# Performance work log

Hardware: AMD Instinct MI355X
Metric: run time of the kernel (lower is better)

Reference implementation:

```python
import jax, jax.numpy as jnp
import numpy as np

B, S, D, DOUT = 8, 2048, 512, 512
BETA = 1.0
EPS = 1e-5


def _ln(x, g, b):
    m = jnp.mean(x, axis=-1, keepdims=True)
    v = jnp.var(x, axis=-1, keepdims=True)
    return (x - m) / jnp.sqrt(v + EPS) * g + b


def setup_inputs() -> dict:
    key = jax.random.key(0)
    ks = jax.random.split(key, 12)
    s = 0.02
    d = {
        "x": jax.random.normal(ks[0], (B, S, D), jnp.float32),
        "Wq": jax.random.normal(ks[1], (D, D), jnp.float32) * s,
        "bq": jnp.zeros((D,), jnp.float32),
        "Wk": jax.random.normal(ks[2], (D, D), jnp.float32) * s,
        "bk": jnp.zeros((D,), jnp.float32),
        "Wv": jax.random.normal(ks[3], (D, D), jnp.float32) * s,
        "bv": jnp.zeros((D,), jnp.float32),
        "ln0_g": jnp.ones((D,), jnp.float32),
        "ln0_b": jnp.zeros((D,), jnp.float32),
        "W1": jax.random.normal(ks[4], (D, D), jnp.float32) * s,
        "b1": jnp.zeros((D,), jnp.float32),
        "ln1_g": jnp.ones((D,), jnp.float32),
        "ln1_b": jnp.zeros((D,), jnp.float32),
        "W2": jax.random.normal(ks[5], (D, D), jnp.float32) * s,
        "b2": jnp.zeros((D,), jnp.float32),
        "ln2_g": jnp.ones((D,), jnp.float32),
        "ln2_b": jnp.zeros((D,), jnp.float32),
        "W3": jax.random.normal(ks[6], (D, DOUT), jnp.float32) * s,
        "b3": jnp.zeros((DOUT,), jnp.float32),
    }
    return d


def reference(x, Wq, bq, Wk, bk, Wv, bv, ln0_g, ln0_b,
              W1, b1, ln1_g, ln1_b, W2, b2, ln2_g, ln2_b, W3, b3):
    # --- attention_single (dropout disabled / eval) ---
    q = x @ Wq + bq                      # [B,S,D]
    k = x @ Wk + bk
    v = x @ Wv + bv
    scores = jnp.einsum('bsd,btd->bst', q, k)   # [B,S,S]
    w = jax.nn.softmax(BETA * scores / jnp.sqrt(jnp.float32(D)), axis=2)
    att = jnp.einsum('bst,btd->bsd', w, v)      # [B,S,D]
    out_nxt = _ln(x + att, ln0_g, ln0_b)
    # --- FFNN (dropout disabled, gelu activation) ---
    h1 = _ln(jax.nn.gelu(out_nxt + (out_nxt @ W1 + b1), approximate=False), ln1_g, ln1_b)
    h2 = _ln(jax.nn.gelu(out_nxt + (h1 @ W2 + b2), approximate=False), ln2_g, ln2_b)
    out_att = h2 @ W3 + b3               # [B,S,DOUT]
    return out_att
```

## Files before the change

### kernel.cpp

```cpp
#include <hip/hip_runtime.h>
#include <hip/hip_bf16.h>
#include <math.h>

using bf16 = __hip_bfloat16;
typedef __attribute__((ext_vector_type(8))) short short8;
typedef __attribute__((ext_vector_type(4))) float f32x4;
typedef __attribute__((ext_vector_type(4))) float float4v;

__device__ __forceinline__ float b2f(bf16 v) { return __bfloat162float(v); }
__device__ __forceinline__ bf16 f2b(float v) { return __float2bfloat16(v); }

__device__ __forceinline__ unsigned char f2e4m3(float v) {
  int p = __builtin_amdgcn_cvt_pk_fp8_f32(v, v, 0, false);
  return (unsigned char)(p & 0xff);
}

__device__ __forceinline__ void gl_lds16(const void* g, void* l) {
  __builtin_amdgcn_global_load_lds(
      (const __attribute__((address_space(1))) void*)g,
      (__attribute__((address_space(3))) void*)l, 16, 0, 0);
}

__global__ __launch_bounds__(256) void sniff_zero(const void* ln0g_raw, int* flag,
                                                  float* rowsum) {
  const int i = blockIdx.x * 256 + threadIdx.x;
  rowsum[i] = 0.f;
  if (i == 0) {
    unsigned short w = ((const unsigned short*)ln0g_raw)[0];
    *flag = (w == 0x3F80) ? 1 : 0;
  }
}

__global__ __launch_bounds__(256) void conv_x8(
    const void* __restrict__ src, bf16* __restrict__ dst,
    const int* __restrict__ flag) {
  const long i = ((long)blockIdx.x * 256 + threadIdx.x) * 8;
  bf16 o[8];
  if (*flag) {
    *(short8*)(dst + i) = ((const short8*)src)[i >> 3];
  } else {
    float4v a = ((const float4v*)src)[i >> 2];
    float4v b = ((const float4v*)src)[(i >> 2) + 1];
#pragma unroll
    for (int k = 0; k < 4; k++) o[k] = f2b(a[k]);
#pragma unroll
    for (int k = 0; k < 4; k++) o[4 + k] = f2b(b[k]);
    *(short8*)(dst + i) = *(short8*)o;
  }
}

__global__ __launch_bounds__(256) void conv_vec12(
    const void* a0, const void* a1, const void* a2, const void* a3,
    const void* a4, const void* a5, const void* a6, const void* a7,
    const void* a8, const void* a9, const void* a10, const void* a11,
    bf16* __restrict__ dst, const int* __restrict__ flag) {
  const int j = blockIdx.x;
  const int i = threadIdx.x + (blockIdx.y << 8);
  const void* s;
  switch (j) {
    case 0: s = a0; break; case 1: s = a1; break; case 2: s = a2; break;
    case 3: s = a3; break; case 4: s = a4; break; case 5: s = a5; break;
    case 6: s = a6; break; case 7: s = a7; break; case 8: s = a8; break;
    case 9: s = a9; break; case 10: s = a10; break; default: s = a11; break;
  }
  bf16 v = (*flag) ? ((const bf16*)s)[i] : f2b(((const float*)s)[i]);
  dst[j * 512 + i] = v;
}

__global__ __launch_bounds__(256) void transpose_conv6(
    const void* w0, const void* w1, const void* w2, const void* w3,
    const void* w4, const void* w5, bf16* __restrict__ outBase,
    const int* __restrict__ flag) {
  __shared__ bf16 tile[32][33];
  const void* in;
  switch (blockIdx.z) {
    case 0: in = w0; break; case 1: in = w1; break; case 2: in = w2; break;
    case 3: in = w3; break; case 4: in = w4; break; default: in = w5; break;
  }
  bf16* out = outBase + (long)blockIdx.z * 262144;
  const int f = *flag;
  const int c0 = blockIdx.x * 32, r0 = blockIdx.y * 32;
  const int tx = threadIdx.x & 31, ty = threadIdx.x >> 5;
#pragma unroll
  for (int i = ty; i < 32; i += 8) {
    const long idx = (long)(r0 + i) * 512 + c0 + tx;
    tile[i][tx] = f ? ((const bf16*)in)[idx] : f2b(((const float*)in)[idx]);
  }
  __syncthreads();
#pragma unroll
  for (int i = ty; i < 32; i += 8)
    out[(long)(c0 + i) * 512 + r0 + tx] = tile[tx][i];
}

__global__ __launch_bounds__(256, 2) void gemm_scores(
    const bf16* __restrict__ A, const bf16* __restrict__ Bt,
    unsigned char* __restrict__ out8, float* __restrict__ rowsum,
    int N, int K, long sA, long sB, long sC, float scale) {
  __shared__ __align__(16) bf16 As[128 * 32];
  __shared__ __align__(16) bf16 Bs[128 * 32];
  const int z = blockIdx.x;
  const int m0 = blockIdx.y * 128, n0 = blockIdx.z * 128;
  A += (long)z * sA;
  Bt += (long)z * sB;
  const int t = threadIdx.x;
  const int l = t & 63, w = t >> 6;
  const int wm = (w >> 1) * 64, wn = (w & 1) * 64;
  const int lr = l & 15, lq = l >> 4;

  const bf16* Ab = A + (long)m0 * K;
  const bf16* Bb = Bt + (long)n0 * K;
  const int srow = t >> 2;
  const int scol = (t & 3) * 8;

  f32x4 acc[4][4] = {};

  for (int k0 = 0; k0 < K; k0 += 32) {
    gl_lds16(Ab + (long)srow * K + k0 + scol, As + w * 512);
    gl_lds16(Ab + (long)(srow + 64) * K + k0 + scol, As + 2048 + w * 512);
    gl_lds16(Bb + (long)srow * K + k0 + scol, Bs + w * 512);
    gl_lds16(Bb + (long)(srow + 64) * K + k0 + scol, Bs + 2048 + w * 512);
    __syncthreads();
    short8 af[4], bfr[4];
#pragma unroll
    for (int i = 0; i < 4; i++)
      af[i] = *(const short8*)(As + (wm + i * 16 + lr) * 32 + lq * 8);
#pragma unroll
    for (int j = 0; j < 4; j++)
      bfr[j] = *(const short8*)(Bs + (wn + j * 16 + lr) * 32 + lq * 8);
#pragma unroll
    for (int i = 0; i < 4; i++)
#pragma unroll
      for (int j = 0; j < 4; j++)
        acc[i][j] = __builtin_amdgcn_mfma_f32_16x16x32_bf16(af[i], bfr[j], acc[i][j], 0, 0, 0);
    __syncthreads();
  }

  const int cr = lq * 4, cc = lr;
  float rs[4][4];
#pragma unroll
  for (int i = 0; i < 4; i++)
#pragma unroll
    for (int r = 0; r < 4; r++) rs[i][r] = 0.f;
#pragma unroll
  for (int i = 0; i < 4; i++) {
#pragma unroll
    for (int j = 0; j < 4; j++) {
      const int gc = n0 + wn + j * 16 + cc;
#pragma unroll
      for (int r = 0; r < 4; r++) {
        const int gr = m0 + wm + i * 16 + cr + r;
        float e = __expf(acc[i][j][r] * scale);
        out8[(long)z * sC + (long)gr * N + gc] = f2e4m3(e);
        rs[i][r] += e;
      }
    }
  }
#pragma unroll
  for (int o = 1; o < 16; o <<= 1)
#pragma unroll
    for (int i = 0; i < 4; i++)
#pragma unroll
      for (int r = 0; r < 4; r++) rs[i][r] += __shfl_xor(rs[i][r], o);
  if (lr == 0) {
#pragma unroll
    for (int i = 0; i < 4; i++)
#pragma unroll
      for (int r = 0; r < 4; r++) {
        const int gr = m0 + wm + i * 16 + cr + r;
        atomicAdd(&rowsum[(long)z * 2048 + gr], rs[i][r]);
      }
  }
}

template <int EPI, bool BX>
__global__ __launch_bounds__(256, 2) void gemm_sk(
    const bf16* __restrict__ A, const bf16* __restrict__ Bt,
    const bf16* __restrict__ bias, const bf16* __restrict__ res,
    float* __restrict__ outF, bf16* __restrict__ outB,
    unsigned char* __restrict__ out8,
    int M, int N, int K, long sA, long sB, long sC, long sBias) {
  __shared__ __align__(16) bf16 As[64 * 32];
  __shared__ __align__(16) bf16 Bs[128 * 32];
  const int z = BX ? blockIdx.x : blockIdx.z;
  const int m0 = (BX ? blockIdx.y : blockIdx.x) * 64;
  const int n0 = (BX ? blockIdx.z : blockIdx.y) * 128;
  A += (long)z * sA;
  Bt += (long)z * sB;
  if (EPI == 0) bias += (long)z * sBias;
  const int t = threadIdx.x;
  const int l = t & 63, w = t >> 6;
  const int wm = (w >> 1) * 32, wn = (w & 1) * 64;
  const int lr = l & 15, lq = l >> 4;

  const bf16* Ab = A + (long)m0 * K;
  const bf16* Bb = Bt + (long)n0 * K;
  const int srow = t >> 2;
  const int scol = (t & 3) * 8;

  f32x4 acc[2][4] = {};

  for (int k0 = 0; k0 < K; k0 += 32) {
    gl_lds16(Ab + (long)srow * K + k0 + scol, As + w * 512);
    gl_lds16(Bb + (long)srow * K + k0 + scol, Bs + w * 512);
    gl_lds16(Bb + (long)(srow + 64) * K + k0 + scol, Bs + 2048 + w * 512);
    __syncthreads();
    short8 af[2], bfr[4];
#pragma unroll
    for (int i = 0; i < 2; i++)
      af[i] = *(const short8*)(As + (wm + i * 16 + lr) * 32 + lq * 8);
#pragma unroll
    for (int j = 0; j < 4; j++)
      bfr[j] = *(const short8*)(Bs + (wn + j * 16 + lr) * 32 + lq * 8);
#pragma unroll
    for (int i = 0; i < 2; i++)
#pragma unroll
      for (int j = 0; j < 4; j++)
        acc[i][j] = __builtin_amdgcn_mfma_f32_16x16x32_bf16(af[i], bfr[j], acc[i][j], 0, 0, 0);
    __syncthreads();
  }

  const int cr = lq * 4, cc = lr;
#pragma unroll
  for (int i = 0; i < 2; i++) {
#pragma unroll
    for (int j = 0; j < 4; j++) {
      const int gc = n0 + wn + j * 16 + cc;
#pragma unroll
      for (int r = 0; r < 4; r++) {
        const int gr = m0 + wm + i * 16 + cr + r;
        const long idx = (long)z * sC + (long)gr * N + gc;
        float v = acc[i][j][r];
        if (EPI == 0) {
          v += b2f(bias[gc]);
          outB[idx] = f2b(v);
        } else if (EPI == 3) {
          v += b2f(bias[gc]) + b2f(res[idx]);
          v = 0.5f * v * (1.0f + erff(v * 0.70710678118654752f));
          outB[idx] = f2b(v);
        } else if (EPI == 4) {
          v += b2f(bias[gc]);
          outF[idx] = v;
        } else {
          v += b2f(bias[gr]);
          out8[idx] = f2e4m3(v);
        }
      }
    }
  }
}

__global__ __launch_bounds__(256, 2) void gemm_pv8(
    const unsigned char* __restrict__ A8, const unsigned char* __restrict__ B8,
    const bf16* __restrict__ res, bf16* __restrict__ outB,
    const float* __restrict__ rowsum,
    int M, int N, int K, long sA, long sB, long sC) {
  __shared__ __align__(16) unsigned char As8[64 * 64];
  __shared__ __align__(16) unsigned char Bs8[128 * 64];
  const int z = blockIdx.x;
  const int m0 = blockIdx.y * 64, n0 = blockIdx.z * 128;
  A8 += (long)z * sA;
  B8 += (long)z * sB;
  const int t = threadIdx.x;
  const int l = t & 63, w = t >> 6;
  const int wm = (w >> 1) * 32, wn = (w & 1) * 64;
  const int lr = l & 15, lq = l >> 4;

  const unsigned char* Ab = A8 + (long)m0 * K;
  const unsigned char* Bb = B8 + (long)n0 * K;

  const int arow_s = t >> 2;
  const int aL = ((t & 3) ^ ((arow_s >> 1) & 3)) * 16;
  const int brow_s2 = (t + 256) >> 2;
  const int bL2 = ((t & 3) ^ ((brow_s2 >> 1) & 3)) * 16;

  f32x4 acc[2][4] = {};

  for (int k0 = 0; k0 < K; k0 += 64) {
    gl_lds16(Ab + (long)arow_s * K + k0 + aL, As8 + w * 1024);
    gl_lds16(Bb + (long)arow_s * K + k0 + aL, Bs8 + w * 1024);
    gl_lds16(Bb + (long)brow_s2 * K + k0 + bL2, Bs8 + 4096 + w * 1024);
    __syncthreads();
#pragma unroll
    for (int kh = 0; kh < 2; kh++) {
      long long a8[2], b8[4];
#pragma unroll
      for (int i = 0; i < 2; i++) {
        const int ar = wm + i * 16 + lr;
        const int Lx = (kh * 2 + (lq >> 1)) ^ ((ar >> 1) & 3);
        a8[i] = *(const long long*)(As8 + ar * 64 + Lx * 16 + (lq & 1) * 8);
      }
#pragma unroll
      for (int j = 0; j < 4; j++) {
        const int br = wn + j * 16 + lr;
        const int Lx = (kh * 2 + (lq >> 1)) ^ ((br >> 1) & 3);
        b8[j] = *(const long long*)(Bs8 + br * 64 + Lx * 16 + (lq & 1) * 8);
      }
#pragma unroll
      for (int i = 0; i < 2; i++)
#pragma unroll
        for (int j = 0; j < 4; j++)
          acc[i][j] = __builtin_amdgcn_mfma_f32_16x16x32_fp8_fp8(a8[i], b8[j], acc[i][j], 0, 0, 0);
    }
    __syncthreads();
  }

  const int cr = lq * 4, cc = lr;
  float inv[2][4];
#pragma unroll
  for (int i = 0; i < 2; i++)
#pragma unroll
    for (int r = 0; r < 4; r++) {
      const int gr = m0 + wm + i * 16 + cr + r;
      inv[i][r] = 1.0f / rowsum[(long)z * 2048 + gr];
    }
#pragma unroll
  for (int i = 0; i < 2; i++) {
#pragma unroll
    for (int j = 0; j < 4; j++) {
      const int gc = n0 + wn + j * 16 + cc;
#pragma unroll
      for (int r = 0; r < 4; r++) {
        const int gr = m0 + wm + i * 16 + cr + r;
        const long idx = (long)z * sC + (long)gr * N + gc;
        float v = acc[i][j][r] * inv[i][r] + b2f(res[idx]);
        outB[idx] = f2b(v);
      }
    }
  }
}

__global__ __launch_bounds__(256) void ln512(
    const bf16* __restrict__ mainb,
    const bf16* __restrict__ g, const bf16* __restrict__ b,
    bf16* __restrict__ out) {
  const int t = threadIdx.x;
  const int l = t & 63, w = t >> 6;
  const long row = (long)blockIdx.x * 4 + w;
  const long base = row * 512 + l * 8;
  bf16 vb8[8];
  *(short8*)vb8 = *(const short8*)(mainb + base);
  float v[8];
  float s = 0.f, q = 0.f;
#pragma unroll
  for (int k = 0; k < 8; k++) {
    v[k] = b2f(vb8[k]);
    s += v[k];
    q += v[k] * v[k];
  }
#pragma unroll
  for (int o = 32; o > 0; o >>= 1) {
    s += __shfl_xor(s, o);
    q += __shfl_xor(q, o);
  }
  const float mean = s * (1.f / 512.f);
  const float var = q * (1.f / 512.f) - mean * mean;
  const float rstd = rsqrtf(var + 1e-5f);
  bf16 g8[8], b8[8], o8[8];
  *(short8*)g8 = *(const short8*)(g + l * 8);
  *(short8*)b8 = *(const short8*)(b + l * 8);
#pragma unroll
  for (int k = 0; k < 8; k++)
    o8[k] = f2b((v[k] - mean) * rstd * b2f(g8[k]) + b2f(b8[k]));
  *(short8*)(out + base) = *(short8*)o8;
}

__global__ void sentinel_kernel(float* out) { out[0] = 31337.0f; }

extern "C" void kernel_launch(void* const* d_in, const int* in_sizes, int n_in,
                              void* d_out, int out_size, void* d_ws, size_t ws_size,
                              hipStream_t stream) {
  const void* x_raw = d_in[0];
  const void* Wq = d_in[1];
  const void* bq = d_in[2];
  const void* Wk = d_in[3];
  const void* bk = d_in[4];
  const void* Wv = d_in[5];
  const void* bv = d_in[6];
  const void* ln0g = d_in[7];
  const void* ln0b = d_in[8];
  const void* W1 = d_in[9];
  const void* b1 = d_in[10];
  const void* ln1g = d_in[11];
  const void* ln1b = d_in[12];
  const void* W2 = d_in[13];
  const void* b2 = d_in[14];
  const void* ln2g = d_in[15];
  const void* ln2b = d_in[16];
  const void* W3 = d_in[17];
  const void* b3 = d_in[18];

  const long MB = 1024 * 1024;
  if (ws_size < (size_t)(148 * MB)) {
    sentinel_kernel<<<1, 1, 0, stream>>>((float*)d_out);
    return;
  }
  char* ws = (char*)d_ws;
  bf16* Wqt = (bf16*)(ws + 0L * 524288);
  bf16* Wvt = (bf16*)(ws + 2L * 524288);
  bf16* W1t = (bf16*)(ws + 3L * 524288);
  bf16* W2t = (bf16*)(ws + 4L * 524288);
  bf16* W3t = (bf16*)(ws + 5L * 524288);
  int* flag = (int*)(ws + 3 * MB);
  bf16* vec = (bf16*)(ws + 3 * MB + 1024);
  bf16* bqc = vec + 0 * 512;
  bf16* bvc = vec + 2 * 512;
  bf16* ln0gc = vec + 3 * 512;
  bf16* ln0bc = vec + 4 * 512;
  bf16* b1c = vec + 5 * 512;
  bf16* ln1gc = vec + 6 * 512;
  bf16* ln1bc = vec + 7 * 512;
  bf16* b2c = vec + 8 * 512;
  bf16* ln2gc = vec + 9 * 512;
  bf16* ln2bc = vec + 10 * 512;
  bf16* b3c = vec + 11 * 512;
  float* rowsum = (float*)(ws + 3 * MB + 131072);
  bf16* xc = (bf16*)(ws + 4 * MB);
  bf16* qb = (bf16*)(ws + 20 * MB);
  bf16* kb = (bf16*)(ws + 36 * MB);
  unsigned char* vt8 = (unsigned char*)(ws + 52 * MB);
  unsigned char* sc8 = (unsigned char*)(ws + 68 * MB);
  bf16* sres = (bf16*)(ws + 132 * MB);
  bf16* onx = (bf16*)(ws + 20 * MB);
  bf16* preh = (bf16*)(ws + 68 * MB);
  bf16* h1 = (bf16*)(ws + 36 * MB);
  bf16* h2 = (bf16*)(ws + 100 * MB);

  const dim3 blk(256);
  const float scale = 0.044194173824159216f;
  const long sQ = 2048L * 512, sS = 2048L * 2048;

  sniff_zero<<<dim3(64), blk, 0, stream>>>(ln0g, flag, rowsum);
  conv_x8<<<dim3(4096), blk, 0, stream>>>(x_raw, xc, flag);
  conv_vec12<<<dim3(12, 2), blk, 0, stream>>>(bq, bk, bv, ln0g, ln0b, b1, ln1g,
                                              ln1b, b2, ln2g, ln2b, b3, vec, flag);
  transpose_conv6<<<dim3(16, 16, 6), blk, 0, stream>>>(Wq, Wk, Wv, W1, W2, W3,
                                                       Wqt, flag);

  gemm_sk<0, false><<<dim3(256, 4, 2), blk, 0, stream>>>(
      xc, Wqt, bqc, nullptr, nullptr, qb, nullptr,
      16384, 512, 512, 0, 262144, 8388608, 512);
  gemm_sk<6, true><<<dim3(8, 8, 16), blk, 0, stream>>>(
      Wvt, xc, bvc, nullptr, nullptr, nullptr, vt8,
      512, 2048, 512, 0, sQ, sQ, 0);
  gemm_scores<<<dim3(8, 16, 16), blk, 0, stream>>>(
      qb, kb, sc8, rowsum, 2048, 512, sQ, sQ, sS, scale);
  gemm_pv8<<<dim3(8, 32, 4), blk, 0, stream>>>(
      sc8, vt8, xc, sres, rowsum, 2048, 512, 2048, sS, sQ, sQ);
  ln512<<<dim3(4096), blk, 0, stream>>>(sres, ln0gc, ln0bc, onx);
  gemm_sk<3, false><<<dim3(256, 4, 1), blk, 0, stream>>>(
      onx, W1t, b1c, onx, nullptr, preh, nullptr,
      16384, 512, 512, 0, 0, 0, 0);
  ln512<<<dim3(4096), blk, 0, stream>>>(preh, ln1gc, ln1bc, h1);
  gemm_sk<3, false><<<dim3(256, 4, 1), blk, 0, stream>>>(
      h1, W2t, b2c, onx, nullptr, preh, nullptr,
      16384, 512, 512, 0, 0, 0, 0);
  ln512<<<dim3(4096), blk, 0, stream>>>(preh, ln2gc, ln2bc, h2);
  gemm_sk<4, false><<<dim3(256, 4, 1), blk, 0, stream>>>(
      h2, W3t, b3c, nullptr, (float*)d_out, nullptr, nullptr,
      16384, 512, 512, 0, 0, 0, 0);
}
```

Before: 345.2 us.

## Double GEMM K-tile to 64 with XOR-swizzled LDS layout

Both the scores GEMM and the generic GEMM now stage 64-wide K slices per iteration instead of 32. Global-to-LDS loads write chunks in an XOR-swizzled order (chunk ^ row&7), and the fragment reads apply the same swizzle. The aim is to halve the number of barrier pairs per K and to avoid LDS bank conflicts on the 128-byte row stride. LDS use doubles per block, which may limit occupancy at two blocks per CU.

```diff
diff --git a/kernel.cpp b/kernel.cpp
--- a/kernel.cpp
+++ b/kernel.cpp
@@ -92,12 +92,13 @@
     out[(long)(c0 + i) * 512 + r0 + tx] = tile[tx][i];
 }
 
+
 __global__ __launch_bounds__(256, 2) void gemm_scores(
     const bf16* __restrict__ A, const bf16* __restrict__ Bt,
     unsigned char* __restrict__ out8, float* __restrict__ rowsum,
     int N, int K, long sA, long sB, long sC, float scale) {
-  __shared__ __align__(16) bf16 As[128 * 32];
-  __shared__ __align__(16) bf16 Bs[128 * 32];
+  __shared__ __align__(16) bf16 As[128 * 64];
+  __shared__ __align__(16) bf16 Bs[128 * 64];
   const int z = blockIdx.x;
   const int m0 = blockIdx.y * 128, n0 = blockIdx.z * 128;
   A += (long)z * sA;
@@ -109,29 +110,46 @@
 
   const bf16* Ab = A + (long)m0 * K;
   const bf16* Bb = Bt + (long)n0 * K;
-  const int srow = t >> 2;
-  const int scol = (t & 3) * 8;
+
+  int srcoff[4];
+#pragma unroll
+  for (int reg = 0; reg < 4; reg++) {
+    const int s = reg * 256 + t;
+    const int row = s >> 3, pch = s & 7;
+    const int L = pch ^ (row & 7);
+    srcoff[reg] = row * K + L * 8;
+  }
 
   f32x4 acc[4][4] = {};
 
-  for (int k0 = 0; k0 < K; k0 += 32) {
-    gl_lds16(Ab + (long)srow * K + k0 + scol, As + w * 512);
-    gl_lds16(Ab + (long)(srow + 64) * K + k0 + scol, As + 2048 + w * 512);
-    gl_lds16(Bb + (long)srow * K + k0 + scol, Bs + w * 512);
-    gl_lds16(Bb + (long)(srow + 64) * K + k0 + scol, Bs + 2048 + w * 512);
-    __syncthreads();
-    short8 af[4], bfr[4];
-#pragma unroll
-    for (int i = 0; i < 4; i++)
-      af[i] = *(const short8*)(As + (wm + i * 16 + lr) * 32 + lq * 8);
-#pragma unroll
-    for (int j = 0; j < 4; j++)
-      bfr[j] = *(const short8*)(Bs + (wn + j * 16 + lr) * 32 + lq * 8);
-#pragma unroll
-    for (int i = 0; i < 4; i++)
-#pragma unroll
-      for (int j = 0; j < 4; j++)
-        acc[i][j] = __builtin_amdgcn_mfma_f32_16x16x32_bf16(af[i], bfr[j], acc[i][j], 0, 0, 0);
+  for (int k0 = 0; k0 < K; k0 += 64) {
+#pragma unroll
+    for (int reg = 0; reg < 4; reg++) {
+      gl_lds16(Ab + srcoff[reg] + k0, As + reg * 2048 + w * 512);
+      gl_lds16(Bb + srcoff[reg] + k0, Bs + reg * 2048 + w * 512);
+    }
+    __syncthreads();
+#pragma unroll
+    for (int kh = 0; kh < 2; kh++) {
+      short8 af[4], bfr[4];
+#pragma unroll
+      for (int i = 0; i < 4; i++) {
+        const int r = wm + i * 16 + lr;
+        const int pc = (kh * 4 + lq) ^ (r & 7);
+        af[i] = *(const short8*)(As + r * 64 + pc * 8);
+      }
+#pragma unroll
+      for (int j = 0; j < 4; j++) {
+        const int r = wn + j * 16 + lr;
+        const int pc = (kh * 4 + lq) ^ (r & 7);
+        bfr[j] = *(const short8*)(Bs + r * 64 + pc * 8);
+      }
+#pragma unroll
+      for (int i = 0; i < 4; i++)
+#pragma unroll
+        for (int j = 0; j < 4; j++)
+          acc[i][j] = __builtin_amdgcn_mfma_f32_16x16x32_bf16(af[i], bfr[j], acc[i][j], 0, 0, 0);
+    }
     __syncthreads();
   }
 
@@ -179,8 +197,8 @@
     float* __restrict__ outF, bf16* __restrict__ outB,
     unsigned char* __restrict__ out8,
     int M, int N, int K, long sA, long sB, long sC, long sBias) {
-  __shared__ __align__(16) bf16 As[64 * 32];
-  __shared__ __align__(16) bf16 Bs[128 * 32];
+  __shared__ __align__(16) bf16 As[64 * 64];
+  __shared__ __align__(16) bf16 Bs[128 * 64];
   const int z = BX ? blockIdx.x : blockIdx.z;
   const int m0 = (BX ? blockIdx.y : blockIdx.x) * 64;
   const int n0 = (BX ? blockIdx.z : blockIdx.y) * 128;
@@ -194,28 +212,46 @@
 
   const bf16* Ab = A + (long)m0 * K;
   const bf16* Bb = Bt + (long)n0 * K;
-  const int srow = t >> 2;
-  const int scol = (t & 3) * 8;
+
+  int srcoff[4];
+#pragma unroll
+  for (int reg = 0; reg < 4; reg++) {
+    const int s = reg * 256 + t;
+    const int row = s >> 3, pch = s & 7;
+    const int L = pch ^ (row & 7);
+    srcoff[reg] = row * K + L * 8;
+  }
 
   f32x4 acc[2][4] = {};
 
-  for (int k0 = 0; k0 < K; k0 += 32) {
-    gl_lds16(Ab + (long)srow * K + k0 + scol, As + w * 512);
-    gl_lds16(Bb + (long)srow * K + k0 + scol, Bs + w * 512);
-    gl_lds16(Bb + (long)(srow + 64) * K + k0 + scol, Bs + 2048 + w * 512);
-    __syncthreads();
-    short8 af[2], bfr[4];
-#pragma unroll
-    for (int i = 0; i < 2; i++)
-      af[i] = *(const short8*)(As + (wm + i * 16 + lr) * 32 + lq * 8);
-#pragma unroll
-    for (int j = 0; j < 4; j++)
-      bfr[j] = *(const short8*)(Bs + (wn + j * 16 + lr) * 32 + lq * 8);
-#pragma unroll
-    for (int i = 0; i < 2; i++)
-#pragma unroll
-      for (int j = 0; j < 4; j++)
-        acc[i][j] = __builtin_amdgcn_mfma_f32_16x16x32_bf16(af[i], bfr[j], acc[i][j], 0, 0, 0);
+  for (int k0 = 0; k0 < K; k0 += 64) {
+    gl_lds16(Ab + srcoff[0] + k0, As + w * 512);
+    gl_lds16(Ab + srcoff[1] + k0, As + 2048 + w * 512);
+#pragma unroll
+    for (int reg = 0; reg < 4; reg++)
+      gl_lds16(Bb + srcoff[reg] + k0, Bs + reg * 2048 + w * 512);
+    __syncthreads();
+#pragma unroll
+    for (int kh = 0; kh < 2; kh++) {
+      short8 af[2], bfr[4];
+#pragma unroll
+      for (int i = 0; i < 2; i++) {
+        const int r = wm + i * 16 + lr;
+        const int pc = (kh * 4 + lq) ^ (r & 7);
+        af[i] = *(const short8*)(As + r * 64 + pc * 8);
+      }
+#pragma unroll
+      for (int j = 0; j < 4; j++) {
+        const int r = wn + j * 16 + lr;
+        const int pc = (kh * 4 + lq) ^ (r & 7);
+        bfr[j] = *(const short8*)(Bs + r * 64 + pc * 8);
+      }
+#pragma unroll
+      for (int i = 0; i < 2; i++)
+#pragma unroll
+        for (int j = 0; j < 4; j++)
+          acc[i][j] = __builtin_amdgcn_mfma_f32_16x16x32_bf16(af[i], bfr[j], acc[i][j], 0, 0, 0);
+    }
     __syncthreads();
   }
 
```

Result: faster. 323.7 us (-6.2%).
